# Optimization experiments

Measured on AMD Instinct MI355X. Metric: run time of the kernel, lower is better.

The kernel has to match this reference:

```python
import jax, jax.numpy as jnp
import numpy as np

D = 1024
K = 256
B = 8192


def setup_inputs() -> dict:
    key = jax.random.key(0)
    kx, kw, kd, kp = jax.random.split(key, 4)
    x = jax.random.normal(kx, (B, D), dtype=jnp.float32)
    # scale weights ~1/sqrt(d) so the 11-matmul chain stays numerically sane
    Ws = jax.random.normal(kw, (10, D, D), dtype=jnp.float32) / jnp.sqrt(jnp.float32(D))
    W_dec = jax.random.normal(kd, (D, K), dtype=jnp.float32) / jnp.sqrt(jnp.float32(K))
    perm = jax.random.randint(kp, (K,), 0, D, dtype=jnp.int64)
    return {"x": x, "Ws": Ws, "W_dec": W_dec, "perm": perm}


def reference(x, Ws, W_dec, perm):
    # torch nn.Linear(d,d,bias=False): y = x @ W.T
    # source applies fc1..fc9, then fc9 AGAIN, then fc10 (11 matmuls, 10 weights)
    order = list(range(9)) + [8, 9]
    h = x
    for i in order:
        h = h @ Ws[i].T  # [B, D]
    y = h[:, perm]        # vectorized gather, replaces per-row python loop [B, K]
    out = y @ W_dec.T     # fc_decode: [B, D]
    return out
```

## Files before the change

### kernel.cpp

```cpp
#include <hip/hip_runtime.h>
#include <stdint.h>
#include <stddef.h>

typedef __bf16 bf16;
typedef __bf16 bf16x8 __attribute__((ext_vector_type(8)));
typedef float f32x4 __attribute__((ext_vector_type(4)));

__device__ __forceinline__ void global_to_lds16(const void* g, void* l) {
  const __attribute__((address_space(1))) unsigned* gp =
      reinterpret_cast<const __attribute__((address_space(1))) unsigned*>(
          reinterpret_cast<uintptr_t>(g));
  __attribute__((address_space(3))) unsigned* lp =
      reinterpret_cast<__attribute__((address_space(3))) unsigned*>(
          reinterpret_cast<uintptr_t>(l));
  __builtin_amdgcn_global_load_lds(gp, lp, 16, 0, 0);
}

template <typename OutT>
__device__ __forceinline__ void gemm128_body(const bf16* __restrict__ A,
                                             const bf16* __restrict__ B,
                                             OutT* __restrict__ C,
                                             int bx, int by) {
  __shared__ bf16 As[128 * 32];
  __shared__ bf16 Bs[128 * 32];

  const int tid = threadIdx.x;
  const int wave = tid >> 6, lane = tid & 63;
  const int quad = lane >> 4, l16 = lane & 15;
  const int rowBase = by * 128;
  const int colBase = bx * 128;
  const int waveM = (wave >> 1) * 64, waveN = (wave & 1) * 64;

  const int e = tid * 8;
  const int sr = e >> 5, sc = e & 31;
  const bf16* Ag0 = A + (size_t)(rowBase + sr) * 1024 + sc;
  const bf16* Ag1 = Ag0 + (size_t)64 * 1024;
  const bf16* Bg0 = B + (size_t)(colBase + sr) * 1024 + sc;
  const bf16* Bg1 = Bg0 + (size_t)64 * 1024;
  char* AsB0 = (char*)As + wave * 1024;
  char* AsB1 = AsB0 + 4096;
  char* BsB0 = (char*)Bs + wave * 1024;
  char* BsB1 = BsB0 + 4096;

  f32x4 acc[4][4] = {};

  for (int k0 = 0; k0 < 1024; k0 += 32) {
    global_to_lds16(Ag0 + k0, AsB0);
    global_to_lds16(Ag1 + k0, AsB1);
    global_to_lds16(Bg0 + k0, BsB0);
    global_to_lds16(Bg1 + k0, BsB1);
    __syncthreads();
    bf16x8 af[4], bfr[4];
#pragma unroll
    for (int mi = 0; mi < 4; mi++)
      af[mi] = *(const bf16x8*)(As + (waveM + mi * 16 + l16) * 32 + quad * 8);
#pragma unroll
    for (int ni = 0; ni < 4; ni++)
      bfr[ni] = *(const bf16x8*)(Bs + (waveN + ni * 16 + l16) * 32 + quad * 8);
#pragma unroll
    for (int mi = 0; mi < 4; mi++)
#pragma unroll
      for (int ni = 0; ni < 4; ni++)
        acc[mi][ni] = __builtin_amdgcn_mfma_f32_16x16x32_bf16(af[mi], bfr[ni],
                                                              acc[mi][ni], 0, 0, 0);
    __syncthreads();
  }

  OutT* Cb = C + (size_t)(rowBase + waveM) * 1024 + colBase + waveN;
#pragma unroll
  for (int mi = 0; mi < 4; mi++)
#pragma unroll
    for (int ni = 0; ni < 4; ni++)
#pragma unroll
      for (int r = 0; r < 4; r++)
        Cb[(size_t)(mi * 16 + quad * 4 + r) * 1024 + ni * 16 + l16] =
            (OutT)acc[mi][ni][r];
}

struct PrepArgs {
  const float* cvt_src[5]; bf16* cvt_dst[5];
  const float* tr_src[6];  bf16* tr_dst[6];
  const float* Wdec; const int* praw; bf16* Gbf;
};

__global__ __launch_bounds__(256) void prep_all(PrepArgs p) {
  __shared__ alignas(16) char smem[64 * 65 * 2];
  const int b = blockIdx.x;
  const int tid = threadIdx.x;

  if (b < 2560) {
    const int m = b >> 9, blk = b & 511;
    const float* __restrict__ src = p.cvt_src[m];
    bf16* __restrict__ dst = p.cvt_dst[m];
    const int i = (blk * 256 + tid) * 8;
    float4 a = *(const float4*)(src + i);
    float4 c = *(const float4*)(src + i + 4);
    bf16x8 o;
    o[0] = (bf16)a.x; o[1] = (bf16)a.y; o[2] = (bf16)a.z; o[3] = (bf16)a.w;
    o[4] = (bf16)c.x; o[5] = (bf16)c.y; o[6] = (bf16)c.z; o[7] = (bf16)c.w;
    *(bf16x8*)(dst + i) = o;
  } else if (b < 4096) {
    const int t = b - 2560;
    const int m = t >> 8, r = t & 255;
    const float* __restrict__ src = p.tr_src[m];
    bf16* __restrict__ dst = p.tr_dst[m];
    bf16(*tile)[65] = reinterpret_cast<bf16(*)[65]>(smem);
    const int bx = (r & 15) * 64;
    const int by = (r >> 4) * 64;
    const int tx = tid & 63;
    const int ty4 = tid >> 6;
#pragma unroll
    for (int rr = 0; rr < 16; rr++) {
      int row = ty4 * 16 + rr;
      tile[row][tx] = (bf16)src[(size_t)(by + row) * 1024 + bx + tx];
    }
    __syncthreads();
#pragma unroll
    for (int rr = 0; rr < 16; rr++) {
      int row = ty4 * 16 + rr;
      dst[(size_t)(bx + row) * 1024 + by + tx] = tile[tx][row];
    }
  } else {
    const int j = b - 4096;
    float* row = (float*)smem;
    int* perm_l = (int*)(smem + 4096);
    int* nzp = (int*)(smem + 4096 + 1024);
#pragma unroll
    for (int c = 0; c < 4; c++) row[tid * 4 + c] = 0.f;
    if (tid == 0) *nzp = 0;
    __syncthreads();
    if (tid < 128 && p.praw[2 * tid + 1] != 0) atomicOr(nzp, 1);
    __syncthreads();
    const int is64 = (*nzp == 0);
    perm_l[tid] = is64 ? p.praw[2 * tid] : p.praw[tid];
    __syncthreads();
    atomicAdd(&row[perm_l[tid]], p.Wdec[(size_t)j * 256 + tid]);
    __syncthreads();
#pragma unroll
    for (int c = 0; c < 4; c++)
      p.Gbf[(size_t)j * 1024 + tid * 4 + c] = (bf16)row[tid * 4 + c];
  }
}

struct L1Args {
  const bf16* A[6]; const bf16* B[6]; bf16* C[6];
  const float* x; bf16* xbf;
};

__global__ __launch_bounds__(256) void l1_gemm_xcvt(L1Args a) {
  const int b = blockIdx.x;
  if (b < 384) {
    const int z = b >> 6, t = b & 63;
    gemm128_body<bf16>(a.A[z], a.B[z], a.C[z], t & 7, t >> 3);
  } else {
    const int i = ((b - 384) * 256 + (int)threadIdx.x) * 8;
    float4 v0 = *(const float4*)(a.x + i);
    float4 v1 = *(const float4*)(a.x + i + 4);
    bf16x8 o;
    o[0] = (bf16)v0.x; o[1] = (bf16)v0.y; o[2] = (bf16)v0.z; o[3] = (bf16)v0.w;
    o[4] = (bf16)v1.x; o[5] = (bf16)v1.y; o[6] = (bf16)v1.z; o[7] = (bf16)v1.w;
    *(bf16x8*)(a.xbf + i) = o;
  }
}

struct GemmBatch { const bf16* A[3]; const bf16* B[3]; bf16* C[3]; };

__global__ __launch_bounds__(256) void tree_gemm(GemmBatch bt) {
  const int b = blockIdx.x;
  const int z = b >> 6, t = b & 63;
  gemm128_body<bf16>(bt.A[z], bt.B[z], bt.C[z], t & 7, t >> 3);
}

__global__ __launch_bounds__(256) void final_gemm(const bf16* __restrict__ A,
                                                  const bf16* __restrict__ B,
                                                  float* __restrict__ C) {
  gemm128_body<float>(A, B, C, blockIdx.x, blockIdx.y);
}

extern "C" void kernel_launch(void* const* d_in, const int* in_sizes, int n_in,
                              void* d_out, int out_size, void* d_ws, size_t ws_size,
                              hipStream_t stream) {
  const float* x    = (const float*)d_in[0];
  const float* Wsrc = (const float*)d_in[1];
  const float* Wdec = (const float*)d_in[2];
  const int*   praw = (const int*)d_in[3];
  float* out = (float*)d_out;

  constexpr size_t MAT  = 1024ull * 1024ull;
  constexpr size_t SLOT = 2ull * 1024 * 1024;

  char* ws = (char*)d_ws;
  bf16* Wrm[5];
  for (int i = 0; i < 5; i++) Wrm[i] = (bf16*)(ws + (size_t)i * SLOT);
  bf16* Wt[6];
  for (int i = 0; i < 6; i++) Wt[i] = (bf16*)(ws + (size_t)(5 + i) * SLOT);
  bf16* Gbf = (bf16*)(ws + 11 * SLOT);
  bf16* xbf = (bf16*)(ws + 12 * SLOT);
  bf16* P[6];
  for (int i = 0; i < 6; i++) P[i] = (bf16*)(ws + (size_t)(20 + i) * SLOT);
  bf16* Q[3];
  for (int i = 0; i < 3; i++) Q[i] = (bf16*)(ws + (size_t)(26 + i) * SLOT);
  bf16* Rb = (bf16*)(ws + 29 * SLOT);
  bf16* Fb = (bf16*)(ws + 30 * SLOT);

  PrepArgs pa;
  const int rmIdx[5] = {1, 3, 5, 7, 8};
  for (int i = 0; i < 5; i++) { pa.cvt_src[i] = Wsrc + (size_t)rmIdx[i] * MAT; pa.cvt_dst[i] = Wrm[i]; }
  const int trIdx[6] = {0, 2, 4, 6, 8, 9};
  for (int i = 0; i < 6; i++) { pa.tr_src[i] = Wsrc + (size_t)trIdx[i] * MAT; pa.tr_dst[i] = Wt[i]; }
  pa.Wdec = Wdec; pa.praw = praw; pa.Gbf = Gbf;
  prep_all<<<dim3(5120), 256, 0, stream>>>(pa);

  L1Args l1;
  const bf16* l1a[6] = {Gbf, Wt[4], Wrm[3], Wt[2], Wrm[1], Wt[0]};
  const bf16* l1b[6] = {Wt[5], Wrm[4], Wt[3], Wrm[2], Wt[1], Wrm[0]};
  for (int i = 0; i < 6; i++) { l1.A[i] = l1a[i]; l1.B[i] = l1b[i]; l1.C[i] = P[i]; }
  l1.x = x; l1.xbf = xbf;
  l1_gemm_xcvt<<<dim3(4480), 256, 0, stream>>>(l1);

  GemmBatch L2;
  const bf16* l2a[3] = {P[0], P[3], P[5]};
  const bf16* l2b[3] = {P[1], P[2], P[4]};
  for (int i = 0; i < 3; i++) { L2.A[i] = l2a[i]; L2.B[i] = l2b[i]; L2.C[i] = Q[i]; }
  tree_gemm<<<dim3(192), 256, 0, stream>>>(L2);

  GemmBatch L3{};
  L3.A[0] = Q[0]; L3.B[0] = Q[1]; L3.C[0] = Rb;
  tree_gemm<<<dim3(64), 256, 0, stream>>>(L3);

  GemmBatch L4{};
  L4.A[0] = Rb; L4.B[0] = Q[2]; L4.C[0] = Fb;
  tree_gemm<<<dim3(64), 256, 0, stream>>>(L4);

  final_gemm<<<dim3(8, 64), 256, 0, stream>>>(xbf, Fb, out);

  (void)in_sizes; (void)n_in; (void)out_size; (void)ws_size;
}
```

Baseline: 231.7 us.

## Double K-step per barrier in GEMM and spread x conversion across tree levels

The GEMM body now loads two 32-wide K slices into separate LDS buffers per iteration, which halves the number of barrier pairs per tile. The fp32-to-bf16 conversion of x is moved out of the first tree level and split across levels 2-4, which launch few GEMM blocks and leave the GPU underused. This is meant to fill idle CUs and cut synchronisation overhead, at the cost of doubled LDS use per block and conversion work competing with the GEMM blocks. The conversion units sum to 4096 (1360+1360+1376), which covers all of x.

```diff
diff --git a/kernel.cpp b/kernel.cpp
--- a/kernel.cpp
+++ b/kernel.cpp
@@ -21,8 +21,8 @@
                                              const bf16* __restrict__ B,
                                              OutT* __restrict__ C,
                                              int bx, int by) {
-  __shared__ bf16 As[128 * 32];
-  __shared__ bf16 Bs[128 * 32];
+  __shared__ bf16 As[2][128 * 32];
+  __shared__ bf16 Bs[2][128 * 32];
 
   const int tid = threadIdx.x;
   const int wave = tid >> 6, lane = tid & 63;
@@ -31,38 +31,50 @@
   const int colBase = bx * 128;
   const int waveM = (wave >> 1) * 64, waveN = (wave & 1) * 64;
 
-  const int e = tid * 8;
-  const int sr = e >> 5, sc = e & 31;
+  const int sr = tid >> 2;
+  const int sc = (tid & 3) * 8;
   const bf16* Ag0 = A + (size_t)(rowBase + sr) * 1024 + sc;
   const bf16* Ag1 = Ag0 + (size_t)64 * 1024;
   const bf16* Bg0 = B + (size_t)(colBase + sr) * 1024 + sc;
   const bf16* Bg1 = Bg0 + (size_t)64 * 1024;
-  char* AsB0 = (char*)As + wave * 1024;
-  char* AsB1 = AsB0 + 4096;
-  char* BsB0 = (char*)Bs + wave * 1024;
-  char* BsB1 = BsB0 + 4096;
+
+  char* lA0  = (char*)As[0] + wave * 1024;
+  char* lA0b = lA0 + 4096;
+  char* lA1  = (char*)As[1] + wave * 1024;
+  char* lA1b = lA1 + 4096;
+  char* lB0  = (char*)Bs[0] + wave * 1024;
+  char* lB0b = lB0 + 4096;
+  char* lB1  = (char*)Bs[1] + wave * 1024;
+  char* lB1b = lB1 + 4096;
 
   f32x4 acc[4][4] = {};
 
-  for (int k0 = 0; k0 < 1024; k0 += 32) {
-    global_to_lds16(Ag0 + k0, AsB0);
-    global_to_lds16(Ag1 + k0, AsB1);
-    global_to_lds16(Bg0 + k0, BsB0);
-    global_to_lds16(Bg1 + k0, BsB1);
-    __syncthreads();
-    bf16x8 af[4], bfr[4];
-#pragma unroll
-    for (int mi = 0; mi < 4; mi++)
-      af[mi] = *(const bf16x8*)(As + (waveM + mi * 16 + l16) * 32 + quad * 8);
-#pragma unroll
-    for (int ni = 0; ni < 4; ni++)
-      bfr[ni] = *(const bf16x8*)(Bs + (waveN + ni * 16 + l16) * 32 + quad * 8);
-#pragma unroll
-    for (int mi = 0; mi < 4; mi++)
+  for (int k0 = 0; k0 < 1024; k0 += 64) {
+    global_to_lds16(Ag0 + k0,      lA0);
+    global_to_lds16(Ag1 + k0,      lA0b);
+    global_to_lds16(Ag0 + k0 + 32, lA1);
+    global_to_lds16(Ag1 + k0 + 32, lA1b);
+    global_to_lds16(Bg0 + k0,      lB0);
+    global_to_lds16(Bg1 + k0,      lB0b);
+    global_to_lds16(Bg0 + k0 + 32, lB1);
+    global_to_lds16(Bg1 + k0 + 32, lB1b);
+    __syncthreads();
+#pragma unroll
+    for (int kk = 0; kk < 2; kk++) {
+      bf16x8 af[4], bfr[4];
+#pragma unroll
+      for (int mi = 0; mi < 4; mi++)
+        af[mi] = *(const bf16x8*)(As[kk] + (waveM + mi * 16 + l16) * 32 + quad * 8);
 #pragma unroll
       for (int ni = 0; ni < 4; ni++)
-        acc[mi][ni] = __builtin_amdgcn_mfma_f32_16x16x32_bf16(af[mi], bfr[ni],
-                                                              acc[mi][ni], 0, 0, 0);
+        bfr[ni] = *(const bf16x8*)(Bs[kk] + (waveN + ni * 16 + l16) * 32 + quad * 8);
+#pragma unroll
+      for (int mi = 0; mi < 4; mi++)
+#pragma unroll
+        for (int ni = 0; ni < 4; ni++)
+          acc[mi][ni] = __builtin_amdgcn_mfma_f32_16x16x32_bf16(af[mi], bfr[ni],
+                                                                acc[mi][ni], 0, 0, 0);
+    }
     __syncthreads();
   }
 
@@ -142,18 +154,21 @@
   }
 }
 
-struct L1Args {
+struct TreeArgs {
   const bf16* A[6]; const bf16* B[6]; bf16* C[6];
-  const float* x; bf16* xbf;
+  int nG;
+  const float* x; bf16* xbf; int ubase;
 };
 
-__global__ __launch_bounds__(256) void l1_gemm_xcvt(L1Args a) {
+__global__ __launch_bounds__(256) void tree_level(TreeArgs a) {
   const int b = blockIdx.x;
-  if (b < 384) {
+  const int gBlocks = a.nG * 64;
+  if (b < gBlocks) {
     const int z = b >> 6, t = b & 63;
     gemm128_body<bf16>(a.A[z], a.B[z], a.C[z], t & 7, t >> 3);
   } else {
-    const int i = ((b - 384) * 256 + (int)threadIdx.x) * 8;
+    const int unit = a.ubase + (b - gBlocks);
+    const int i = unit * 2048 + (int)threadIdx.x * 8;
     float4 v0 = *(const float4*)(a.x + i);
     float4 v1 = *(const float4*)(a.x + i + 4);
     bf16x8 o;
@@ -161,14 +176,6 @@
     o[4] = (bf16)v1.x; o[5] = (bf16)v1.y; o[6] = (bf16)v1.z; o[7] = (bf16)v1.w;
     *(bf16x8*)(a.xbf + i) = o;
   }
-}
-
-struct GemmBatch { const bf16* A[3]; const bf16* B[3]; bf16* C[3]; };
-
-__global__ __launch_bounds__(256) void tree_gemm(GemmBatch bt) {
-  const int b = blockIdx.x;
-  const int z = b >> 6, t = b & 63;
-  gemm128_body<bf16>(bt.A[z], bt.B[z], bt.C[z], t & 7, t >> 3);
 }
 
 __global__ __launch_bounds__(256) void final_gemm(const bf16* __restrict__ A,
@@ -211,26 +218,29 @@
   pa.Wdec = Wdec; pa.praw = praw; pa.Gbf = Gbf;
   prep_all<<<dim3(5120), 256, 0, stream>>>(pa);
 
-  L1Args l1;
+  TreeArgs L1{};
   const bf16* l1a[6] = {Gbf, Wt[4], Wrm[3], Wt[2], Wrm[1], Wt[0]};
   const bf16* l1b[6] = {Wt[5], Wrm[4], Wt[3], Wrm[2], Wt[1], Wrm[0]};
-  for (int i = 0; i < 6; i++) { l1.A[i] = l1a[i]; l1.B[i] = l1b[i]; l1.C[i] = P[i]; }
-  l1.x = x; l1.xbf = xbf;
-  l1_gemm_xcvt<<<dim3(4480), 256, 0, stream>>>(l1);
-
-  GemmBatch L2;
+  for (int i = 0; i < 6; i++) { L1.A[i] = l1a[i]; L1.B[i] = l1b[i]; L1.C[i] = P[i]; }
+  L1.nG = 6; L1.x = x; L1.xbf = xbf; L1.ubase = 0;
+  tree_level<<<dim3(384), 256, 0, stream>>>(L1);
+
+  TreeArgs L2{};
   const bf16* l2a[3] = {P[0], P[3], P[5]};
   const bf16* l2b[3] = {P[1], P[2], P[4]};
   for (int i = 0; i < 3; i++) { L2.A[i] = l2a[i]; L2.B[i] = l2b[i]; L2.C[i] = Q[i]; }
-  tree_gemm<<<dim3(192), 256, 0, stream>>>(L2);
-
-  GemmBatch L3{};
+  L2.nG = 3; L2.x = x; L2.xbf = xbf; L2.ubase = 0;
+  tree_level<<<dim3(192 + 1360), 256, 0, stream>>>(L2);
+
+  TreeArgs L3{};
   L3.A[0] = Q[0]; L3.B[0] = Q[1]; L3.C[0] = Rb;
-  tree_gemm<<<dim3(64), 256, 0, stream>>>(L3);
-
-  GemmBatch L4{};
+  L3.nG = 1; L3.x = x; L3.xbf = xbf; L3.ubase = 1360;
+  tree_level<<<dim3(64 + 1360), 256, 0, stream>>>(L3);
+
+  TreeArgs L4{};
   L4.A[0] = Rb; L4.B[0] = Q[2]; L4.C[0] = Fb;
-  tree_gemm<<<dim3(64), 256, 0, stream>>>(L4);
+  L4.nG = 1; L4.x = x; L4.xbf = xbf; L4.ubase = 2720;
+  tree_level<<<dim3(64 + 1376), 256, 0, stream>>>(L4);
 
   final_gemm<<<dim3(8, 64), 256, 0, stream>>>(xbf, Fb, out);
 
```

Measured after the change: 218.0 us. 1.06x faster.
